# Performance work log

Hardware: AMD Instinct MI355X
Metric: run time of the kernel (lower is better)

Reference implementation:

```python
import jax, jax.numpy as jnp
import numpy as np

GRID_MIN, GRID_MAX, GRID_SIZE = -4.0, 4.0, 12
BANDWIDTH = (GRID_MAX - GRID_MIN) / max(GRID_SIZE - 1, 1)  # 8/11


def setup_inputs() -> dict:
    key = jax.random.key(0)
    k1, k2, k3, k4 = jax.random.split(key, 4)
    B, I, O, G = 16384, 512, 512, GRID_SIZE
    x = jax.random.normal(k1, (B, I), dtype=jnp.float32)
    coeff = jax.random.normal(k2, (I, O, G), dtype=jnp.float32) * 0.05
    base_w = jax.random.normal(k3, (O, I), dtype=jnp.float32) * (1.0 / np.sqrt(I))
    base_b = jax.random.normal(k4, (O,), dtype=jnp.float32) * 0.01
    centers = jnp.linspace(GRID_MIN, GRID_MAX, G, dtype=jnp.float32)
    return {"x": x, "coeff": coeff, "base_w": base_w, "base_b": base_b, "centers": centers}


def reference(x, coeff, base_w, base_b, centers):
    # RBF basis: [B, I, G]
    diff = (x[..., None] - centers) / jnp.float32(BANDWIDTH)
    basis = jnp.exp(-0.5 * diff * diff)
    # spline contraction over in_dim and grid: [B, O]
    spline = jnp.einsum('big,iog->bo', basis, coeff)
    # residual base linear (torch Linear: x @ W^T + b)
    return spline + x @ base_w.T + base_b
```

## Files before the change

### kernel.cpp

```cpp
#include <hip/hip_runtime.h>
#include <hip/hip_bf16.h>


#define N_DIM 512
#define I_DIM 512
#define KTOT  6656
#define NSTEP 104

typedef short short8 __attribute__((ext_vector_type(8)));
typedef float f32x16 __attribute__((ext_vector_type(16)));
typedef unsigned int u32x4 __attribute__((ext_vector_type(4)));

#define CVTPK(dst, lo, hi) \
  asm("v_cvt_pk_bf16_f32 %0, %1, %2" : "=v"(dst) : "v"(lo), "v"(hi))

__device__ __forceinline__ unsigned short f2bf(float f) {
  union { float f; unsigned int u; } c; c.f = f;
  unsigned int r = (c.u + 0x7FFFu + ((c.u >> 16) & 1)) >> 16;
  return (unsigned short)r;
}

__global__ __launch_bounds__(256) void prep_w(const float* __restrict__ coeff,
                                              const float* __restrict__ base_w,
                                              unsigned short* __restrict__ Wb2) {
  int t = blockIdx.x * 256 + threadIdx.x;
  int e0 = (t & 1) * 4;
  int go = t >> 1;
  int o  = go & 511;
  int g  = go >> 9;
  int k4 = g * 8 + e0;
  int ic = k4 / 832;
  int rem = k4 - ic * 832;
  int slot = rem >> 6;
  int ii = rem & 63;
  int i = ic * 64 + ii;
  float v0, v1, v2, v3;
  if (slot == 0) {
    const float4 bw = *(const float4*)(base_w + (size_t)o * I_DIM + i);
    v0 = bw.x; v1 = bw.y; v2 = bw.z; v3 = bw.w;
  } else {
    int gg = slot - 1;
    const float* cp = coeff + (size_t)i * (N_DIM * 12) + o * 12 + gg;
    v0 = cp[0]; v1 = cp[6144]; v2 = cp[2 * 6144]; v3 = cp[3 * 6144];
  }
  ushort4 s;
  s.x = f2bf(v0); s.y = f2bf(v1); s.z = f2bf(v2); s.w = f2bf(v3);
  *(ushort4*)(Wb2 + (size_t)go * 8 + e0) = s;
}

__global__ __launch_bounds__(512, 2) void kan_gemm(const float* __restrict__ x,
                                                   const unsigned short* __restrict__ Wb2,
                                                   const float* __restrict__ bias,
                                                   float* __restrict__ out) {
  __shared__ unsigned short Asw[2][8 * 128 * 8];
  __shared__ unsigned short Bsw[3][8 * 256 * 8];

  const int tid  = threadIdx.x;
  const int lane = tid & 63;
  const int wid  = tid >> 6;
  const int wm   = wid >> 2, wn = wid & 3;
  const int l31  = lane & 31, hl = lane >> 5;

  const int rb = blockIdx.x >> 1;
  const int cb = blockIdx.x & 1;
  const int M0 = rb * 128;
  const int N0 = cb * 256;

  const int arow = tid & 127;
  const int kgp  = tid >> 7;
  const float* xg = x + (size_t)(M0 + arow) * I_DIM + kgp * 16;
  const int aoff0 = ((kgp * 2) * 128 + arow) * 16;
  const int aoff1 = ((kgp * 2 + 1) * 128 + arow) * 16;

  const unsigned short* bsrc[4];
  int bdst[4];
#pragma unroll
  for (int q = 0; q < 4; ++q) {
    bsrc[q] = Wb2 + ((size_t)wid * 512 + N0 + q * 64 + lane) * 8;
    bdst[q] = (wid * 256 + q * 64) * 16;
  }

#define STAGE(T_, RING_) do {                                                  \
    const size_t ko_ = (size_t)(T_) * 32768;                                   \
    char* d_ = (char*)&Bsw[RING_][0];                                          \
    _Pragma("unroll")                                                          \
    for (int q_ = 0; q_ < 4; ++q_)                                             \
      __builtin_amdgcn_global_load_lds(                                        \
          (const __attribute__((address_space(1))) void*)(bsrc[q_] + ko_),     \
          (__attribute__((address_space(3))) void*)(d_ + bdst[q_]), 16, 0, 0); \
  } while (0)

  const int aBase = (hl * 128 + wm * 64 + l31) * 16;
  const int bBase = (hl * 256 + wn * 64 + l31) * 16;

  f32x16 acc[2][2];
#pragma unroll
  for (int i = 0; i < 2; ++i)
#pragma unroll
    for (int j = 0; j < 2; ++j)
#pragma unroll
      for (int r = 0; r < 16; ++r) acc[i][j][r] = 0.f;

  float bb[16], ff[16];
  float4 xh[4];

#pragma unroll
  for (int q = 0; q < 4; ++q) xh[q] = *(const float4*)(xg + q * 4);
  STAGE(0, 0);
  STAGE(1, 1);
  {
    float f[16];
#pragma unroll
    for (int q = 0; q < 4; ++q) {
      f[q*4+0] = xh[q].x; f[q*4+1] = xh[q].y; f[q*4+2] = xh[q].z; f[q*4+3] = xh[q].w;
    }
    unsigned int w[8];
#pragma unroll
    for (int j = 0; j < 8; ++j) CVTPK(w[j], f[2*j], f[2*j+1]);
    char* pAe = (char*)&Asw[0][0];
    *(u32x4*)(pAe + aoff0) = (u32x4){w[0], w[1], w[2], w[3]};
    *(u32x4*)(pAe + aoff1) = (u32x4){w[4], w[5], w[6], w[7]};
#pragma unroll
    for (int j = 0; j < 16; ++j) {
      float u = fmaf(f[j], 1.375f, 5.5f);
      bb[j] = exp2f(-0.72134752044448170f * u * u);
      ff[j] = exp2f(fmaf(u, 1.44269504088896340f, -0.72134752044448170f));
    }
  }
  asm volatile("s_waitcnt vmcnt(4) lgkmcnt(0)" ::: "memory");
  __builtin_amdgcn_s_barrier();

  int cur3 = 0, tm13 = 0, cchunk = 1;
#pragma unroll 1
  for (int t = 0; t < NSTEP; ++t) {
    const char* pA  = (const char*)&Asw[t & 1][0];
    const char* pB  = (const char*)&Bsw[cur3][0];
    char*       pAe = (char*)&Asw[(t + 1) & 1][0];

    short8 av[2][4], bv[2][4];
#pragma unroll
    for (int s = 0; s < 4; ++s) {
      av[0][s] = *(const short8*)(pA + aBase + s * 4096);
      av[1][s] = *(const short8*)(pA + aBase + s * 4096 + 512);
      bv[0][s] = *(const short8*)(pB + bBase + s * 8192);
      bv[1][s] = *(const short8*)(pB + bBase + s * 8192 + 512);
    }

    const bool doStage = (t < NSTEP - 2);
    {
      int nring = cur3 + 2; if (nring >= 3) nring -= 3;
      if (doStage) STAGE(t + 2, nring);
    }

    if (t < NSTEP - 1) {
      unsigned int w[8];
      if (tm13 == 12) {
        float f[16];
#pragma unroll
        for (int q = 0; q < 4; ++q) {
          f[q*4+0] = xh[q].x; f[q*4+1] = xh[q].y; f[q*4+2] = xh[q].z; f[q*4+3] = xh[q].w;
        }
#pragma unroll
        for (int j = 0; j < 8; ++j) CVTPK(w[j], f[2*j], f[2*j+1]);
      } else {
#pragma unroll
        for (int j = 0; j < 8; ++j) CVTPK(w[j], bb[2*j], bb[2*j+1]);
      }
      *(u32x4*)(pAe + aoff0) = (u32x4){w[0], w[1], w[2], w[3]};
      *(u32x4*)(pAe + aoff1) = (u32x4){w[4], w[5], w[6], w[7]};
    }

    __builtin_amdgcn_s_setprio(1);
#pragma unroll
    for (int s = 0; s < 4; ++s) {
      acc[0][0] = __builtin_amdgcn_mfma_f32_32x32x16_bf16(av[0][s], bv[0][s], acc[0][0], 0, 0, 0);
      acc[0][1] = __builtin_amdgcn_mfma_f32_32x32x16_bf16(av[0][s], bv[1][s], acc[0][1], 0, 0, 0);
      acc[1][0] = __builtin_amdgcn_mfma_f32_32x32x16_bf16(av[1][s], bv[0][s], acc[1][0], 0, 0, 0);
      acc[1][1] = __builtin_amdgcn_mfma_f32_32x32x16_bf16(av[1][s], bv[1][s], acc[1][1], 0, 0, 0);
    }
    __builtin_amdgcn_s_setprio(0);

    if (t < NSTEP - 2) {
      if (tm13 == 12) {
#pragma unroll
        for (int j = 0; j < 16; ++j) {
          float xv = (j < 4 ? (&xh[0].x)[j] : j < 8 ? (&xh[1].x)[j-4]
                     : j < 12 ? (&xh[2].x)[j-8] : (&xh[3].x)[j-12]);
          float u = fmaf(xv, 1.375f, 5.5f);
          bb[j] = exp2f(-0.72134752044448170f * u * u);
          ff[j] = exp2f(fmaf(u, 1.44269504088896340f, -0.72134752044448170f));
        }
      } else if (tm13 != 11) {
#pragma unroll
        for (int j = 0; j < 16; ++j) {
          bb[j] *= ff[j];
          ff[j] *= 0.36787944117144233f;
        }
      }
    }
    bool xstep = (tm13 == 2) && (cchunk < 8);
    if (xstep) {
      const float* xn = xg + (size_t)cchunk * 64;
#pragma unroll
      for (int q = 0; q < 4; ++q) xh[q] = *(const float4*)(xn + q * 4);
      ++cchunk;
    }

    if (!doStage) {
      asm volatile("s_waitcnt vmcnt(0) lgkmcnt(0)" ::: "memory");
    } else if (xstep) {
      asm volatile("s_waitcnt vmcnt(8) lgkmcnt(0)" ::: "memory");
    } else {
      asm volatile("s_waitcnt vmcnt(4) lgkmcnt(0)" ::: "memory");
    }
    __builtin_amdgcn_s_barrier();

    if (++tm13 == 13) tm13 = 0;
    cur3 = (cur3 == 2) ? 0 : cur3 + 1;
  }

  float bvv[2];
#pragma unroll
  for (int fo = 0; fo < 2; ++fo) bvv[fo] = bias[N0 + wn * 64 + fo * 32 + l31];
  const int rbase = 4 * hl;
#pragma unroll
  for (int fb = 0; fb < 2; ++fb) {
#pragma unroll
    for (int fo = 0; fo < 2; ++fo) {
      const size_t cix = (size_t)(N0 + wn * 64 + fo * 32 + l31);
#pragma unroll
      for (int r = 0; r < 16; ++r) {
        int row = M0 + wm * 64 + fb * 32 + (r & 3) + 8 * (r >> 2) + rbase;
        out[(size_t)row * N_DIM + cix] = acc[fb][fo][r] + bvv[fo];
      }
    }
  }
}

extern "C" void kernel_launch(void* const* d_in, const int* in_sizes, int n_in,
                              void* d_out, int out_size, void* d_ws, size_t ws_size,
                              hipStream_t stream) {
  const float* x      = (const float*)d_in[0];
  const float* coeff  = (const float*)d_in[1];
  const float* base_w = (const float*)d_in[2];
  const float* base_b = (const float*)d_in[3];
  unsigned short* Wb2 = (unsigned short*)d_ws;

  prep_w<<<3328, 256, 0, stream>>>(coeff, base_w, Wb2);
  kan_gemm<<<256, 512, 0, stream>>>(x, Wb2, base_b, (float*)d_out);
}
```

Before: 157.2 us.

## Load B fragments directly from global memory and remap blocks across XCDs

Drops the three-stage LDS ring buffer for the weight operand. Each wave now reads its B fragments straight from global memory into registers at the start of every step, with no async prefetch. The block index is also remapped so that blocks on the same XCD share a column half and neighbouring row tiles, which should improve L2 reuse of the weights. This frees LDS and removes the wait-count bookkeeping, but global-load latency is now exposed every iteration without software pipelining, and the explicit setprio and waitcnt tuning is gone.

```diff
diff --git a/kernel.cpp b/kernel.cpp
--- a/kernel.cpp
+++ b/kernel.cpp
@@ -53,7 +53,6 @@
                                                    const float* __restrict__ bias,
                                                    float* __restrict__ out) {
   __shared__ unsigned short Asw[2][8 * 128 * 8];
-  __shared__ unsigned short Bsw[3][8 * 256 * 8];
 
   const int tid  = threadIdx.x;
   const int lane = tid & 63;
@@ -61,10 +60,12 @@
   const int wm   = wid >> 2, wn = wid & 3;
   const int l31  = lane & 31, hl = lane >> 5;
 
-  const int rb = blockIdx.x >> 1;
-  const int cb = blockIdx.x & 1;
-  const int M0 = rb * 128;
-  const int N0 = cb * 256;
+  const int bid = blockIdx.x;
+  const int xcd = bid & 7, jj = bid >> 3;
+  const int cb  = xcd >> 2;
+  const int rb  = jj * 4 + (xcd & 3);
+  const int M0  = rb * 128;
+  const int N0  = cb * 256;
 
   const int arow = tid & 127;
   const int kgp  = tid >> 7;
@@ -72,26 +73,15 @@
   const int aoff0 = ((kgp * 2) * 128 + arow) * 16;
   const int aoff1 = ((kgp * 2 + 1) * 128 + arow) * 16;
 
-  const unsigned short* bsrc[4];
-  int bdst[4];
-#pragma unroll
-  for (int q = 0; q < 4; ++q) {
-    bsrc[q] = Wb2 + ((size_t)wid * 512 + N0 + q * 64 + lane) * 8;
-    bdst[q] = (wid * 256 + q * 64) * 16;
-  }
-
-#define STAGE(T_, RING_) do {                                                  \
-    const size_t ko_ = (size_t)(T_) * 32768;                                   \
-    char* d_ = (char*)&Bsw[RING_][0];                                          \
-    _Pragma("unroll")                                                          \
-    for (int q_ = 0; q_ < 4; ++q_)                                             \
-      __builtin_amdgcn_global_load_lds(                                        \
-          (const __attribute__((address_space(1))) void*)(bsrc[q_] + ko_),     \
-          (__attribute__((address_space(3))) void*)(d_ + bdst[q_]), 16, 0, 0); \
-  } while (0)
+  const char* Wb = (const char*)Wb2;
+  int boff[4][2];
+#pragma unroll
+  for (int s = 0; s < 4; ++s)
+#pragma unroll
+    for (int fo = 0; fo < 2; ++fo)
+      boff[s][fo] = (((s * 2 + hl) * 512) + N0 + wn * 64 + fo * 32 + l31) * 16;
 
   const int aBase = (hl * 128 + wm * 64 + l31) * 16;
-  const int bBase = (hl * 256 + wn * 64 + l31) * 16;
 
   f32x16 acc[2][2];
 #pragma unroll
@@ -103,11 +93,9 @@
 
   float bb[16], ff[16];
   float4 xh[4];
-
 #pragma unroll
   for (int q = 0; q < 4; ++q) xh[q] = *(const float4*)(xg + q * 4);
-  STAGE(0, 0);
-  STAGE(1, 1);
+
   {
     float f[16];
 #pragma unroll
@@ -127,34 +115,31 @@
       ff[j] = exp2f(fmaf(u, 1.44269504088896340f, -0.72134752044448170f));
     }
   }
-  asm volatile("s_waitcnt vmcnt(4) lgkmcnt(0)" ::: "memory");
-  __builtin_amdgcn_s_barrier();
-
-  int cur3 = 0, tm13 = 0, cchunk = 1;
-#pragma unroll 1
+  __syncthreads();
+
+  int eslot = 1, cchunk = 0;
   for (int t = 0; t < NSTEP; ++t) {
     const char* pA  = (const char*)&Asw[t & 1][0];
-    const char* pB  = (const char*)&Bsw[cur3][0];
     char*       pAe = (char*)&Asw[(t + 1) & 1][0];
-
-    short8 av[2][4], bv[2][4];
+    const char* WbT = Wb + (size_t)t * 65536;
+
+    short8 bv[4][2];
 #pragma unroll
     for (int s = 0; s < 4; ++s) {
-      av[0][s] = *(const short8*)(pA + aBase + s * 4096);
-      av[1][s] = *(const short8*)(pA + aBase + s * 4096 + 512);
-      bv[0][s] = *(const short8*)(pB + bBase + s * 8192);
-      bv[1][s] = *(const short8*)(pB + bBase + s * 8192 + 512);
-    }
-
-    const bool doStage = (t < NSTEP - 2);
-    {
-      int nring = cur3 + 2; if (nring >= 3) nring -= 3;
-      if (doStage) STAGE(t + 2, nring);
+      bv[s][0] = *(const short8*)(WbT + boff[s][0]);
+      bv[s][1] = *(const short8*)(WbT + boff[s][1]);
+    }
+
+    short8 av[4][2];
+#pragma unroll
+    for (int s = 0; s < 4; ++s) {
+      av[s][0] = *(const short8*)(pA + aBase + s * 4096);
+      av[s][1] = *(const short8*)(pA + aBase + s * 4096 + 512);
     }
 
     if (t < NSTEP - 1) {
       unsigned int w[8];
-      if (tm13 == 12) {
+      if (eslot == 0) {
         float f[16];
 #pragma unroll
         for (int q = 0; q < 4; ++q) {
@@ -162,61 +147,43 @@
         }
 #pragma unroll
         for (int j = 0; j < 8; ++j) CVTPK(w[j], f[2*j], f[2*j+1]);
-      } else {
-#pragma unroll
-        for (int j = 0; j < 8; ++j) CVTPK(w[j], bb[2*j], bb[2*j+1]);
-      }
-      *(u32x4*)(pAe + aoff0) = (u32x4){w[0], w[1], w[2], w[3]};
-      *(u32x4*)(pAe + aoff1) = (u32x4){w[4], w[5], w[6], w[7]};
-    }
-
-    __builtin_amdgcn_s_setprio(1);
-#pragma unroll
-    for (int s = 0; s < 4; ++s) {
-      acc[0][0] = __builtin_amdgcn_mfma_f32_32x32x16_bf16(av[0][s], bv[0][s], acc[0][0], 0, 0, 0);
-      acc[0][1] = __builtin_amdgcn_mfma_f32_32x32x16_bf16(av[0][s], bv[1][s], acc[0][1], 0, 0, 0);
-      acc[1][0] = __builtin_amdgcn_mfma_f32_32x32x16_bf16(av[1][s], bv[0][s], acc[1][0], 0, 0, 0);
-      acc[1][1] = __builtin_amdgcn_mfma_f32_32x32x16_bf16(av[1][s], bv[1][s], acc[1][1], 0, 0, 0);
-    }
-    __builtin_amdgcn_s_setprio(0);
-
-    if (t < NSTEP - 2) {
-      if (tm13 == 12) {
+        *(u32x4*)(pAe + aoff0) = (u32x4){w[0], w[1], w[2], w[3]};
+        *(u32x4*)(pAe + aoff1) = (u32x4){w[4], w[5], w[6], w[7]};
 #pragma unroll
         for (int j = 0; j < 16; ++j) {
-          float xv = (j < 4 ? (&xh[0].x)[j] : j < 8 ? (&xh[1].x)[j-4]
-                     : j < 12 ? (&xh[2].x)[j-8] : (&xh[3].x)[j-12]);
-          float u = fmaf(xv, 1.375f, 5.5f);
+          float u = fmaf(f[j], 1.375f, 5.5f);
           bb[j] = exp2f(-0.72134752044448170f * u * u);
           ff[j] = exp2f(fmaf(u, 1.44269504088896340f, -0.72134752044448170f));
         }
-      } else if (tm13 != 11) {
+      } else {
+#pragma unroll
+        for (int j = 0; j < 8; ++j) CVTPK(w[j], bb[2*j], bb[2*j+1]);
+        *(u32x4*)(pAe + aoff0) = (u32x4){w[0], w[1], w[2], w[3]};
+        *(u32x4*)(pAe + aoff1) = (u32x4){w[4], w[5], w[6], w[7]};
 #pragma unroll
         for (int j = 0; j < 16; ++j) {
           bb[j] *= ff[j];
           ff[j] *= 0.36787944117144233f;
         }
       }
-    }
-    bool xstep = (tm13 == 2) && (cchunk < 8);
-    if (xstep) {
-      const float* xn = xg + (size_t)cchunk * 64;
-#pragma unroll
-      for (int q = 0; q < 4; ++q) xh[q] = *(const float4*)(xn + q * 4);
-      ++cchunk;
-    }
-
-    if (!doStage) {
-      asm volatile("s_waitcnt vmcnt(0) lgkmcnt(0)" ::: "memory");
-    } else if (xstep) {
-      asm volatile("s_waitcnt vmcnt(8) lgkmcnt(0)" ::: "memory");
-    } else {
-      asm volatile("s_waitcnt vmcnt(4) lgkmcnt(0)" ::: "memory");
-    }
-    __builtin_amdgcn_s_barrier();
-
-    if (++tm13 == 13) tm13 = 0;
-    cur3 = (cur3 == 2) ? 0 : cur3 + 1;
+      if (eslot == 1 && cchunk < 7) {
+        ++cchunk;
+        const float* xn = xg + (size_t)cchunk * 64;
+#pragma unroll
+        for (int q = 0; q < 4; ++q) xh[q] = *(const float4*)(xn + q * 4);
+      }
+      eslot = (eslot == 12) ? 0 : eslot + 1;
+    }
+
+#pragma unroll
+    for (int s = 0; s < 4; ++s) {
+      acc[0][0] = __builtin_amdgcn_mfma_f32_32x32x16_bf16(av[s][0], bv[s][0], acc[0][0], 0, 0, 0);
+      acc[0][1] = __builtin_amdgcn_mfma_f32_32x32x16_bf16(av[s][0], bv[s][1], acc[0][1], 0, 0, 0);
+      acc[1][0] = __builtin_amdgcn_mfma_f32_32x32x16_bf16(av[s][1], bv[s][0], acc[1][0], 0, 0, 0);
+      acc[1][1] = __builtin_amdgcn_mfma_f32_32x32x16_bf16(av[s][1], bv[s][1], acc[1][1], 0, 0, 0);
+    }
+
+    __syncthreads();
   }
 
   float bvv[2];
```

Result: slower. 188.8 us (+20.1%).
